# Optimization experiments

Hardware: AMD Instinct MI355X
Metric: run time of the kernel (lower is better)

Reference implementation:

```python
import jax, jax.numpy as jnp
import numpy as np

B, T, D_MODEL, N_HEAD = 2, 2048, 1024, 16
HEAD_DIM = D_MODEL // N_HEAD
CHUNK, POLY = 16, 1
SCALE = HEAD_DIM ** -0.5


def alpert_basis(L):
    # poly_order=1: constant + linear Legendre-like columns, L2-normalized per column
    t = jnp.linspace(-1.0, 1.0, L)
    W = jnp.stack([jnp.ones_like(t), t], axis=1)  # [L, 2]
    return W / jnp.linalg.norm(W, axis=0, keepdims=True)


def setup_inputs() -> dict:
    key = jax.random.key(0)
    ks = jax.random.split(key, 10)
    d = D_MODEL
    nrm = lambda k, shape, s=0.02: (jax.random.normal(k, shape, jnp.float32) * s)
    return {
        'x': jax.random.normal(ks[0], (B, T, d), jnp.float32),
        'Wq': nrm(ks[1], (d, d)),
        'Wk': nrm(ks[2], (d, d)),
        'Wv': nrm(ks[3], (d, d)),
        'Wo': nrm(ks[4], (d, d)),
        'gate_w': nrm(ks[5], (d, d)),
        'gate_b': jnp.zeros((d,), jnp.float32),
        'A': nrm(ks[6], (N_HEAD, HEAD_DIM, HEAD_DIM)),
        'jump_scale': jnp.ones((1,), jnp.float32),
        'jump_bias': jnp.zeros((1,), jnp.float32),
        'sink_scalar': nrm(ks[7], (1, N_HEAD, 1, 1)),
        'v_null': nrm(ks[8], (1, N_HEAD, 1, HEAD_DIM)),
    }


def _forward(x, Wq, Wk, Wv, Wo, gate_w, gate_b, A, jump_scale, jump_bias, sink_scalar, v_null):
    Bx, Tx, C = x.shape
    H, Dh = N_HEAD, HEAD_DIM
    NEG = jnp.float32(-1e30)

    def lin(W):  # torch Linear: y = x @ W.T, W is [out, in]
        y = jnp.einsum('btc,dc->btd', x, W)
        return y.reshape(Bx, Tx, H, Dh).transpose(0, 2, 1, 3)  # [B,H,T,Dh]

    q_raw, k_raw, v_val = lin(Wq), lin(Wk), lin(Wv)
    g = jax.nn.sigmoid(jnp.einsum('btc,dc->btd', x, gate_w) + gate_b)
    gate = g.reshape(Bx, Tx, H, Dh).transpose(0, 2, 1, 3)

    # symmetric mean/std normalization (torch std is unbiased -> ddof=1)
    ms = 0.5 * (q_raw.mean(-1, keepdims=True) + k_raw.mean(-1, keepdims=True))
    ss = 0.5 * (jnp.std(q_raw, -1, keepdims=True, ddof=1) + jnp.std(k_raw, -1, keepdims=True, ddof=1))
    q_norm = (q_raw - ms) / (ss + 1e-6)
    k_norm = (k_raw - ms) / (ss + 1e-6)

    # RoPE (half-split variant as in source)
    inv = 1.0 / (10000.0 ** (jnp.arange(0, Dh, 2, dtype=jnp.float32) / Dh))
    fr = jnp.arange(Tx, dtype=jnp.float32)[:, None] * inv[None, :]  # [T, Dh/2]
    cos, sin = jnp.cos(fr)[None, None], jnp.sin(fr)[None, None]

    def rope(z):
        z1, z2 = z[..., 0::2], z[..., 1::2]
        return jnp.concatenate([-z2 * sin + z1 * cos, z1 * sin + z2 * cos], axis=-1)

    S = A - jnp.swapaxes(A, -1, -2)  # skew-symmetric per head
    wedge = lambda z: z + jnp.einsum('bhtd,hde->bhte', z, S)
    q_geo, k_geo = wedge(rope(q_norm)), wedge(rope(k_norm))

    W_b = alpert_basis(CHUNK)  # [L, K]
    N, K, L = Tx // CHUNK, W_b.shape[1], CHUNK
    to_chunks = lambda z: z.reshape(Bx, H, N, L, Dh).transpose(2, 0, 1, 3, 4)  # [N,B,H,L,Dh]
    qx, kx, gx = to_chunks(q_geo), to_chunks(k_geo), to_chunks(gate)

    hist0 = jnp.zeros((Bx, H, N, K, Dh), jnp.float32)
    last0 = jnp.zeros((Bx, H, 1, Dh), jnp.float32)
    idx = jnp.arange(N)

    def step(carry, xs):
        hist, last, i = carry
        q_c, k_c, g_c = xs  # [B,H,L,Dh]
        k_coef = jnp.einsum('bhld,lk->bhkd', k_c, W_b)
        sc = jnp.einsum('bhkd,bhnkd->bhn', k_coef, hist) * SCALE
        sc = jnp.where(idx < i, sc, NEG)  # mask unfilled history slots
        w = jax.nn.softmax(sc, axis=-1)
        retr = jnp.einsum('bhn,bhnkd->bhkd', w, hist)
        q_rec = jnp.einsum('bhkd,lk->bhld', retr, W_b)
        jg = jax.nn.sigmoid(sc.max(-1)[..., None, None] * jump_scale + jump_bias)  # [B,H,1,1]
        inj = jnp.where(i > 0, (1.0 - jg) * last + jg * q_rec, 0.0)
        q_out = jnp.cumsum(g_c * q_c, axis=2) + inj
        hist = hist.at[:, :, i].set(jnp.einsum('bhld,lk->bhkd', q_out, W_b))
        return (hist, q_out[:, :, -1:, :], i + 1), q_out

    _, q_outs = jax.lax.scan(step, (hist0, last0, jnp.int32(0)), (qx, kx, gx))
    Q = q_outs.transpose(1, 2, 0, 3, 4).reshape(Bx, H, Tx, Dh)

    att = jnp.einsum('bhtd,bhsd->bhts', Q, k_geo) * SCALE
    causal = jnp.tril(jnp.ones((Tx, Tx), bool))
    att = jnp.where(causal, att, NEG)
    null = jnp.broadcast_to(sink_scalar, (Bx, H, Tx, 1))
    probs = jax.nn.softmax(jnp.concatenate([att, null], axis=-1), axis=-1)
    out = jnp.einsum('bhts,bhsd->bhtd', probs[..., :Tx], v_val) + probs[..., Tx:] * v_null
    out = out.transpose(0, 2, 1, 3).reshape(Bx, Tx, C)
    return jnp.einsum('btc,dc->btd', out, Wo)


def reference(x, Wq, Wk, Wv, Wo, gate_w, gate_b, A, jump_scale, jump_bias, sink_scalar, v_null):
    return _forward(x, Wq, Wk, Wv, Wo, gate_w, gate_b, A, jump_scale, jump_bias, sink_scalar, v_null)
```

## Files before the change

### kernel.cpp

```cpp
#include <hip/hip_runtime.h>
#include <math.h>

#define NB 2
#define NT 2048
#define NH 16
#define DH 64
#define DM 1024

using bf8   = __attribute__((ext_vector_type(8))) short;
using f32x4 = __attribute__((ext_vector_type(4))) float;

static __device__ __forceinline__ ushort f2bf(float f) {
    union { float f; unsigned u; } c; c.f = f;
    unsigned u = c.u + 0x7FFFu + ((c.u >> 16) & 1u);
    return (ushort)(u >> 16);
}

static __device__ __forceinline__ float wbf(int l, int k) {
    if (k == 0) return 0.25f;
    const float invn = 1.0f / sqrtf(1360.0f / 225.0f);
    return (-1.0f + (2.0f / 15.0f) * (float)l) * invn;
}

__global__ __launch_bounds__(512) void gemm3c_kernel(
    const float* __restrict__ x, const float* __restrict__ Wq,
    const float* __restrict__ Wk, const float* __restrict__ gw,
    const float* __restrict__ gbias,
    float* __restrict__ oq, float* __restrict__ ok, float* __restrict__ og,
    const float* __restrict__ wv, const float* __restrict__ wo,
    ushort* __restrict__ xb, ushort* __restrict__ wb)
{
    __shared__ float As[16][132];
    __shared__ float Bs[16][132];
    if (blockIdx.x >= 768) {
        const int id = (blockIdx.x - 768) * 512 + threadIdx.x;
        const int XQ = (NB * NT * DM) / 4;
        const int WQ = (DM * DM) / 4;
        const float4* src;
        ushort* dst;
        if (id < XQ) {
            src = (const float4*)x + id;
            dst = xb + (size_t)id * 4;
        } else {
            const int r = id - XQ;
            const int wi = r / WQ, off = r % WQ;
            const float* w = (wi == 0) ? wv : wo;
            src = (const float4*)w + off;
            dst = wb + (size_t)wi * DM * DM + (size_t)off * 4;
        }
        const float4 v = *src;
        ushort4 o;
        o.x = f2bf(v.x); o.y = f2bf(v.y); o.z = f2bf(v.z); o.w = f2bf(v.w);
        *(ushort4*)dst = o;
        return;
    }
    const int b = blockIdx.x;
    const int z = b >> 8;
    const int by = (b >> 3) & 31;
    const int bx = b & 7;
    const float* Bw = (z == 0) ? Wq : (z == 1) ? Wk : gw;
    float* C = (z == 0) ? oq : (z == 1) ? ok : og;
    const int tid = threadIdx.x;
    const int tx = tid & 31;
    const int ty = tid >> 5;
    const int row0 = by * 128, col0 = bx * 128;
    const int sr = tid >> 2;
    const int sk = (tid & 3) << 2;
    const float* Ap = x  + (size_t)(row0 + sr) * DM + sk;
    const float* Bp = Bw + (size_t)(col0 + sr) * DM + sk;
    float acc[8][4] = {};
    for (int k0 = 0; k0 < DM; k0 += 16) {
        const float4 av = *(const float4*)(Ap + k0);
        const float4 bv = *(const float4*)(Bp + k0);
        __syncthreads();
        As[sk + 0][sr] = av.x; As[sk + 1][sr] = av.y; As[sk + 2][sr] = av.z; As[sk + 3][sr] = av.w;
        Bs[sk + 0][sr] = bv.x; Bs[sk + 1][sr] = bv.y; Bs[sk + 2][sr] = bv.z; Bs[sk + 3][sr] = bv.w;
        __syncthreads();
        #pragma unroll
        for (int kk = 0; kk < 16; ++kk) {
            const float4 a0 = *(const float4*)&As[kk][ty * 4];
            const float4 a1 = *(const float4*)&As[kk][64 + ty * 4];
            const float4 b0 = *(const float4*)&Bs[kk][tx * 4];
            const float a[8] = {a0.x, a0.y, a0.z, a0.w, a1.x, a1.y, a1.z, a1.w};
            const float bb2[4] = {b0.x, b0.y, b0.z, b0.w};
            #pragma unroll
            for (int i = 0; i < 8; ++i)
                #pragma unroll
                for (int j = 0; j < 4; ++j)
                    acc[i][j] = fmaf(a[i], bb2[j], acc[i][j]);
        }
    }
    #pragma unroll
    for (int i = 0; i < 8; ++i) {
        const int m = row0 + ((i < 4) ? (ty * 4 + i) : (64 + ty * 4 + i - 4));
        const int bb = m >> 11, t = m & 2047;
        #pragma unroll
        for (int j = 0; j < 4; ++j) {
            const int n = col0 + tx * 4 + j;
            float v = acc[i][j];
            if (z == 2) v = 1.0f / (1.0f + __expf(-(v + gbias[n])));
            const int h = n >> 6, dh = n & 63;
            C[(((size_t)(bb * NH + h)) * NT + t) * DH + dh] = v;
        }
    }
}

__global__ __launch_bounds__(256) void gemm_bf16_kernel(
    const ushort* __restrict__ Ab, const ushort* __restrict__ Bb,
    float* __restrict__ Cp)
{
    __shared__ ushort Al[128][40];
    __shared__ ushort Bl[64][40];
    const int tid = threadIdx.x;
    const int l = tid & 63, w = tid >> 6;
    const int wr = w >> 1, wc = w & 1;
    const int lr = l & 15, g = l >> 4;
    const int row0 = blockIdx.y * 128, col0 = blockIdx.x * 64;
    f32x4 acc[4][2];
    #pragma unroll
    for (int mi = 0; mi < 4; ++mi)
        #pragma unroll
        for (int ni = 0; ni < 2; ++ni) acc[mi][ni] = (f32x4){0.f, 0.f, 0.f, 0.f};
    const int sa_row = tid >> 1, sa_half = (tid & 1) * 16;
    const int sb_row = tid >> 2, sb_q = (tid & 3) * 8;
    const ushort* Ap = Ab + (size_t)(row0 + sa_row) * DM + sa_half;
    const ushort* Bp = Bb + (size_t)(col0 + sb_row) * DM + sb_q;
    for (int k0 = 0; k0 < DM; k0 += 32) {
        const uint4 a0 = *(const uint4*)(Ap + k0);
        const uint4 a1 = *(const uint4*)(Ap + k0 + 8);
        const uint4 b0 = *(const uint4*)(Bp + k0);
        __syncthreads();
        *(uint4*)&Al[sa_row][sa_half]     = a0;
        *(uint4*)&Al[sa_row][sa_half + 8] = a1;
        *(uint4*)&Bl[sb_row][sb_q]        = b0;
        __syncthreads();
        bf8 a[4], b[2];
        #pragma unroll
        for (int mi = 0; mi < 4; ++mi) a[mi] = *(const bf8*)&Al[wr * 64 + mi * 16 + lr][g * 8];
        #pragma unroll
        for (int ni = 0; ni < 2; ++ni) b[ni] = *(const bf8*)&Bl[wc * 32 + ni * 16 + lr][g * 8];
        #pragma unroll
        for (int mi = 0; mi < 4; ++mi)
            #pragma unroll
            for (int ni = 0; ni < 2; ++ni)
                acc[mi][ni] = __builtin_amdgcn_mfma_f32_16x16x32_bf16(a[mi], b[ni], acc[mi][ni], 0, 0, 0);
    }
    #pragma unroll
    for (int mi = 0; mi < 4; ++mi) {
        const int m0 = row0 + wr * 64 + mi * 16 + g * 4;
        #pragma unroll
        for (int ni = 0; ni < 2; ++ni) {
            const int n = col0 + wc * 32 + ni * 16 + lr;
            #pragma unroll
            for (int r = 0; r < 4; ++r)
                Cp[(size_t)(m0 + r) * DM + n] = acc[mi][ni][r];
        }
    }
}

__global__ __launch_bounds__(256) void nrw_kernel(
    const float* __restrict__ qraw, const float* __restrict__ kraw,
    const float* __restrict__ Amat, float* __restrict__ gateq,
    ushort* __restrict__ kgb,
    float* __restrict__ kcoefA, float* __restrict__ R0A,
    float* __restrict__ R1A, float* __restrict__ r15A)
{
    __shared__ float S[64][64];
    __shared__ float zq[4][64];
    __shared__ float zk[4][64];
    const int bh = blockIdx.x;
    const int h = bh & (NH - 1);
    const int tid = threadIdx.x;
    const int g = tid >> 6, lane = tid & 63;
    for (int idx = tid; idx < 4096; idx += 256) {
        const int d = idx >> 6, e = idx & 63;
        S[d][e] = Amat[(size_t)h * 4096 + d * 64 + e] - Amat[(size_t)h * 4096 + e * 64 + d];
    }
    __syncthreads();
    const int j = lane & 31;
    const float invf = powf(10000.0f, -(float)(2 * j) * (1.0f / 64.0f));
    const int t0 = blockIdx.y * 64 + g * 16;
    float kc0 = 0.f, kc1 = 0.f, run = 0.f, Ra0 = 0.f, Ra1 = 0.f;
    for (int r = 0; r < 16; ++r) {
        const int t = t0 + r;
        const size_t base = ((size_t)bh * NT + t) * DH;
        const float qv = qraw[base + lane];
        const float kv = kraw[base + lane];
        float sq = qv, sk = kv, qq = qv * qv, kk2 = kv * kv;
        #pragma unroll
        for (int off = 32; off; off >>= 1) {
            sq += __shfl_xor(sq, off);
            sk += __shfl_xor(sk, off);
            qq += __shfl_xor(qq, off);
            kk2 += __shfl_xor(kk2, off);
        }
        const float mq = sq * (1.0f / 64.0f), mk = sk * (1.0f / 64.0f);
        const float vq = (qq - 64.0f * mq * mq) * (1.0f / 63.0f);
        const float vk = (kk2 - 64.0f * mk * mk) * (1.0f / 63.0f);
        const float ms = 0.5f * (mq + mk);
        const float ss = 0.5f * (sqrtf(fmaxf(vq, 0.0f)) + sqrtf(fmaxf(vk, 0.0f)));
        const float rinv = 1.0f / (ss + 1e-6f);
        const float qn = (qv - ms) * rinv;
        const float kn = (kv - ms) * rinv;
        const float q1 = __shfl(qn, 2 * j), q2 = __shfl(qn, 2 * j + 1);
        const float k1 = __shfl(kn, 2 * j), k2 = __shfl(kn, 2 * j + 1);
        float sn, cs;
        sincosf((float)t * invf, &sn, &cs);
        const float rq = (lane < 32) ? (q1 * cs - q2 * sn) : (q1 * sn + q2 * cs);
        const float rk = (lane < 32) ? (k1 * cs - k2 * sn) : (k1 * sn + k2 * cs);
        zq[g][lane] = rq;
        zk[g][lane] = rk;
        float aq = 0.0f, ak = 0.0f;
        #pragma unroll 8
        for (int d = 0; d < 64; ++d) {
            const float sde = S[d][lane];
            aq = fmaf(zq[g][d], sde, aq);
            ak = fmaf(zk[g][d], sde, ak);
        }
        const float qgv = rq + aq;
        const float kgv = rk + ak;
        const float gv = gateq[base + lane];
        const float qgpv = gv * qgv;
        gateq[base + lane] = qgpv;
        kgb[base + lane] = f2bf(kgv);
        kc0 = fmaf(kgv, 0.25f, kc0);
        kc1 = fmaf(kgv, wbf(r, 1), kc1);
        run += qgpv;
        Ra0 = fmaf(run, 0.25f, Ra0);
        Ra1 = fmaf(run, wbf(r, 1), Ra1);
    }
    const int unit = bh * 128 + blockIdx.y * 4 + g;
    kcoefA[(size_t)unit * 128 + lane] = kc0;
    kcoefA[(size_t)unit * 128 + 64 + lane] = kc1;
    R0A[(size_t)unit * 64 + lane] = Ra0;
    R1A[(size_t)unit * 64 + lane] = Ra1;
    r15A[(size_t)unit * 64 + lane] = run;
}

__global__ __launch_bounds__(256) void scan_vgemm_kernel(
    const float* __restrict__ kcoefA, const float* __restrict__ R0A,
    const float* __restrict__ R1A, const float* __restrict__ r15A,
    const float* __restrict__ jscale, const float* __restrict__ jbias,
    float* __restrict__ r0O, float* __restrict__ r1O,
    float* __restrict__ lpO, float* __restrict__ jgO,
    const ushort* __restrict__ xb, const ushort* __restrict__ Wb,
    ushort* __restrict__ Vt)
{
    __shared__ char smem[100864];
    if (blockIdx.x >= 32) {
        const int gi = blockIdx.x - 32;
        const int col0 = (gi & 15) * 64;
        const int row0 = (gi >> 4) * 128;
        ushort (*Al)[40] = (ushort(*)[40])smem;
        ushort (*Bl)[40] = (ushort(*)[40])(smem + 10240);
        const int tid = threadIdx.x;
        const int l = tid & 63, w = tid >> 6;
        const int wr = w >> 1, wc = w & 1;
        const int lr = l & 15, g = l >> 4;
        f32x4 acc[4][2];
        #pragma unroll
        for (int mi = 0; mi < 4; ++mi)
            #pragma unroll
            for (int ni = 0; ni < 2; ++ni) acc[mi][ni] = (f32x4){0.f, 0.f, 0.f, 0.f};
        const int sa_row = tid >> 1, sa_half = (tid & 1) * 16;
        const int sb_row = tid >> 2, sb_q = (tid & 3) * 8;
        const ushort* Ap = xb + (size_t)(row0 + sa_row) * DM + sa_half;
        const ushort* Bp = Wb + (size_t)(col0 + sb_row) * DM + sb_q;
        for (int k0 = 0; k0 < DM; k0 += 32) {
            const uint4 a0 = *(const uint4*)(Ap + k0);
            const uint4 a1 = *(const uint4*)(Ap + k0 + 8);
            const uint4 b0 = *(const uint4*)(Bp + k0);
            __syncthreads();
            *(uint4*)&Al[sa_row][sa_half]     = a0;
            *(uint4*)&Al[sa_row][sa_half + 8] = a1;
            *(uint4*)&Bl[sb_row][sb_q]        = b0;
            __syncthreads();
            bf8 a[4], b[2];
            #pragma unroll
            for (int mi = 0; mi < 4; ++mi) a[mi] = *(const bf8*)&Al[wr * 64 + mi * 16 + lr][g * 8];
            #pragma unroll
            for (int ni = 0; ni < 2; ++ni) b[ni] = *(const bf8*)&Bl[wc * 32 + ni * 16 + lr][g * 8];
            #pragma unroll
            for (int mi = 0; mi < 4; ++mi)
                #pragma unroll
                for (int ni = 0; ni < 2; ++ni)
                    acc[mi][ni] = __builtin_amdgcn_mfma_f32_16x16x32_bf16(a[mi], b[ni], acc[mi][ni], 0, 0, 0);
        }
        #pragma unroll
        for (int mi = 0; mi < 4; ++mi) {
            const int m0 = row0 + wr * 64 + mi * 16 + g * 4;
            const int bb = m0 >> 11, t0 = m0 & 2047;
            #pragma unroll
            for (int ni = 0; ni < 2; ++ni) {
                const int n = col0 + wc * 32 + ni * 16 + lr;
                const int h = n >> 6, dh = n & 63;
                ushort4 pk;
                pk.x = f2bf(acc[mi][ni][0]); pk.y = f2bf(acc[mi][ni][1]);
                pk.z = f2bf(acc[mi][ni][2]); pk.w = f2bf(acc[mi][ni][3]);
                *(ushort4*)(Vt + (((size_t)(bb * NH + h)) * DH + dh) * NT + t0) = pk;
            }
        }
        return;
    }
    if (threadIdx.x >= 64) return;
    float* HA  = (float*)smem;
    float* KcL = (float*)(smem + 65536);
    float* EL  = (float*)(smem + 73728);
    float* ET  = (float*)(smem + 82176);
    float* VP  = (float*)(smem + 92416);
    float* mxold = (float*)(smem + 100608);
    float* psold = (float*)(smem + 100672);
    float* pbuf  = (float*)(smem + 100736);
    float* qbuf    = (float*)(smem + 73728);
    float* candBuf = (float*)(smem + 74752);
    const int bh = blockIdx.x;
    const int l = threadIdx.x;
    #pragma unroll
    for (int c = 0; c < 64; ++c)
        *(f32x4*)&HA[c * 256 + l * 4] = (f32x4){0.f, 0.f, 0.f, 0.f};
    const float js = jscale[0], jb = jbias[0];
    const float* kcp  = kcoefA + (size_t)bh * 128 * 128;
    const float* R0p  = R0A  + (size_t)bh * 128 * 64;
    const float* R1p  = R1A  + (size_t)bh * 128 * 64;
    const float* r15p = r15A + (size_t)bh * 128 * 64;
    float* r0o = r0O + (size_t)bh * 128 * 64;
    float* r1o = r1O + (size_t)bh * 128 * 64;
    float* lpo = lpO + (size_t)bh * 128 * 64;
    float* jgo = jgO + (size_t)bh * 128;
    float last = 0.0f;
    const float wb15_1 = wbf(15, 1);
    const int iiq = l >> 2, sq = l & 3;
    const int ch = l >> 2;

    for (int j = 0; j < 8; ++j) {
        const int P = 16 * j;
        #pragma unroll
        for (int t = 0; t < 8; ++t)
            *(f32x4*)&KcL[t * 256 + l * 4] = *(const f32x4*)&kcp[j * 2048 + t * 256 + l * 4];
        float R0b[16], R1b[16], r15b[16];
        #pragma unroll
        for (int t = 0; t < 16; ++t) {
            R0b[t]  = R0p[(P + t) * 64 + l];
            R1b[t]  = R1p[(P + t) * 64 + l];
            r15b[t] = r15p[(P + t) * 64 + l];
        }
        {
            float sA[16], sB[16];
            #pragma unroll
            for (int ii = 0; ii < 16; ++ii) { sA[ii] = 0.f; sB[ii] = 0.f; }
            const int swA = l & 31;
            for (int c = 0; c < 32; ++c) {
                const int cs = ((c ^ swA) << 2);
                const f32x4 hA = *(const f32x4*)&HA[l * 128 + cs];
                const f32x4 hB = *(const f32x4*)&HA[(64 + l) * 128 + cs];
                #pragma unroll
                for (int ii = 0; ii < 16; ++ii) {
                    const f32x4 kc = *(const f32x4*)&KcL[ii * 128 + (c << 2)];
                    sA[ii] = fmaf(hA[0], kc[0], sA[ii]); sA[ii] = fmaf(hA[1], kc[1], sA[ii]);
                    sA[ii] = fmaf(hA[2], kc[2], sA[ii]); sA[ii] = fmaf(hA[3], kc[3], sA[ii]);
                    sB[ii] = fmaf(hB[0], kc[0], sB[ii]); sB[ii] = fmaf(hB[1], kc[1], sB[ii]);
                    sB[ii] = fmaf(hB[2], kc[2], sB[ii]); sB[ii] = fmaf(hB[3], kc[3], sB[ii]);
                }
            }
            #pragma unroll
            for (int ii = 0; ii < 16; ++ii) {
                if (l < P)      EL[ii * 132 + l]      = sA[ii] * 0.125f;
                if (64 + l < P) EL[ii * 132 + 64 + l] = sB[ii] * 0.125f;
            }
        }
        {
            float m = -1e30f;
            for (int n = sq; n < P; n += 4) m = fmaxf(m, EL[iiq * 132 + n]);
            m = fmaxf(m, __shfl_xor(m, 1));
            m = fmaxf(m, __shfl_xor(m, 2));
            if (sq == 0) mxold[iiq] = m;
        }
        {
            const float mo = (P > 0) ? mxold[iiq] : -1e30f;
            float ps = 0.f;
            for (int n = sq; n < P; n += 4) {
                const float e = __expf(EL[iiq * 132 + n] - mo);
                ET[n * 20 + iiq] = e;
                ps += e;
            }
            ps += __shfl_xor(ps, 1);
            ps += __shfl_xor(ps, 2);
            if (sq == 0) psold[iiq] = ps;
        }
        {
            float vp0[16], vp1[16];
            #pragma unroll
            for (int ii = 0; ii < 16; ++ii) { vp0[ii] = 0.f; vp1[ii] = 0.f; }
            for (int n = 0; n < P; ++n) {
                const int sw = n & 31;
                const float h0 = HA[n * 128 + ((ch ^ sw) << 2) + (l & 3)];
                const float h1 = HA[n * 128 + (((16 + ch) ^ sw) << 2) + (l & 3)];
                const f32x4 e0 = *(const f32x4*)&ET[n * 20];
                const f32x4 e1 = *(const f32x4*)&ET[n * 20 + 4];
                const f32x4 e2 = *(const f32x4*)&ET[n * 20 + 8];
                const f32x4 e3 = *(const f32x4*)&ET[n * 20 + 12];
                #pragma unroll
                for (int u = 0; u < 4; ++u) {
                    vp0[u]      = fmaf(e0[u], h0, vp0[u]);      vp1[u]      = fmaf(e0[u], h1, vp1[u]);
                    vp0[4 + u]  = fmaf(e1[u], h0, vp0[4 + u]);  vp1[4 + u]  = fmaf(e1[u], h1, vp1[4 + u]);
                    vp0[8 + u]  = fmaf(e2[u], h0, vp0[8 + u]);  vp1[8 + u]  = fmaf(e2[u], h1, vp1[8 + u]);
                    vp0[12 + u] = fmaf(e3[u], h0, vp0[12 + u]); vp1[12 + u] = fmaf(e3[u], h1, vp1[12 + u]);
                }
            }
            #pragma unroll
            for (int ii = 0; ii < 16; ++ii) {
                VP[ii * 128 + l]      = vp0[ii];
                VP[ii * 128 + 64 + l] = vp1[ii];
            }
        }
        const int n_ = l >> 2, q = l & 3;
        const int qb = l & ~3;
        #pragma unroll
        for (int iL = 0; iL < 16; ++iL) {
            const int i = P + iL;
            const int nrow = P + n_;
            const int nsw = nrow & 31;
            float scp = 0.f;
            #pragma unroll
            for (int c = 0; c < 8; ++c) {
                const f32x4 h  = *(const f32x4*)&HA[nrow * 128 + ((((q << 3) + c) ^ nsw) << 2)];
                const f32x4 kc = *(const f32x4*)&KcL[iL * 128 + (q << 5) + (c << 2)];
                scp = fmaf(h[0], kc[0], scp); scp = fmaf(h[1], kc[1], scp);
                scp = fmaf(h[2], kc[2], scp); scp = fmaf(h[3], kc[3], scp);
            }
            qbuf[l] = scp;
            const float scn = (qbuf[qb] + qbuf[qb + 1]) + (qbuf[qb + 2] + qbuf[qb + 3]);
            const float cand = (n_ < iL) ? scn * 0.125f : -1e30f;
            if (q == 0) candBuf[n_] = cand;
            float m8[8];
            #pragma unroll
            for (int u = 0; u < 8; ++u) m8[u] = fmaxf(candBuf[2 * u], candBuf[2 * u + 1]);
            float m4a = fmaxf(m8[0], m8[1]), m4b = fmaxf(m8[2], m8[3]);
            float m4c = fmaxf(m8[4], m8[5]), m4d = fmaxf(m8[6], m8[7]);
            const float mxn = fmaxf(fmaxf(m4a, m4b), fmaxf(m4c, m4d));
            const float mo = mxold[iL];
            const float mx = fmaxf(mxn, mo);
            const float p = (n_ < iL) ? __expf(cand - mx) : 0.f;
            if (q == 0) pbuf[n_] = p;
            float s8[8];
            #pragma unroll
            for (int u = 0; u < 8; ++u) s8[u] = pbuf[2 * u] + pbuf[2 * u + 1];
            float s4a = s8[0] + s8[1], s4b = s8[2] + s8[3];
            float s4c = s8[4] + s8[5], s4d = s8[6] + s8[7];
            const float psn = (s4a + s4b) + (s4c + s4d);
            float r0 = 0.f, r1 = 0.f;
            if (i > 0) {
                const float so = __expf(mo - mx);
                float racc0 = VP[iL * 128 + l] * so;
                float racc1 = VP[iL * 128 + 64 + l] * so;
                #pragma unroll
                for (int n2 = 0; n2 < iL; ++n2) {
                    const float pn = pbuf[n2];
                    const int nr = P + n2;
                    const int sw2 = nr & 31;
                    racc0 = fmaf(pn, HA[nr * 128 + ((ch ^ sw2) << 2) + (l & 3)], racc0);
                    racc1 = fmaf(pn, HA[nr * 128 + (((16 + ch) ^ sw2) << 2) + (l & 3)], racc1);
                }
                const float ps = fmaf(psold[iL], so, psn);
                const float rden = 1.0f / ps;
                r0 = racc0 * rden;
                r1 = racc1 * rden;
            }
            const float jg = 1.0f / (1.0f + __expf(-fmaf(mx, js, jb)));
            const float lastp = last;
            const float h0n = R0b[iL] + fmaf(jg, r0, 4.0f * (1.0f - jg) * lastp);
            const float h1n = fmaf(jg, r1, R1b[iL]);
            const float qrec15 = fmaf(r0, 0.25f, r1 * wb15_1);
            last = r15b[iL] + fmaf(jg, qrec15, (1.0f - jg) * lastp);
            r0o[i * 64 + l] = r0;
            r1o[i * 64 + l] = r1;
            lpo[i * 64 + l] = lastp;
            if (l == 0) jgo[i] = jg;
            const int swi = i & 31;
            HA[i * 128 + ((ch ^ swi) << 2) + (l & 3)] = h0n;
            HA[i * 128 + (((16 + ch) ^ swi) << 2) + (l & 3)] = h1n;
        }
    }
}

__global__ __launch_bounds__(256) void scan_post_kernel(
    const float* __restrict__ qgp, const float* __restrict__ r0O,
    const float* __restrict__ r1O, const float* __restrict__ lpO,
    const float* __restrict__ jgO, float* __restrict__ Qout)
{
    const int unit = blockIdx.x * 4 + (threadIdx.x >> 6);
    const int d = threadIdx.x & 63;
    const int bh = unit >> 7, i = unit & 127;
    const size_t ub = (size_t)unit * 64 + d;
    const float r0 = r0O[ub], r1 = r1O[ub], lp = lpO[ub];
    const float jg = jgO[unit];
    const size_t cbase = ((size_t)bh * NT + i * 16) * DH + d;
    float run = 0.0f;
    #pragma unroll
    for (int ll = 0; ll < 16; ++ll) {
        run += qgp[cbase + ll * 64];
        const float qrec = fmaf(r0, 0.25f, r1 * wbf(ll, 1));
        const float inj = (i > 0) ? fmaf(jg, qrec, (1.0f - jg) * lp) : 0.0f;
        Qout[cbase + ll * 64] = run + inj;
    }
}

__global__ __launch_bounds__(256) void attn_mfma_kernel(
    const float* __restrict__ Qf, const ushort* __restrict__ Kb,
    const ushort* __restrict__ Vtb, const float* __restrict__ sink,
    const float* __restrict__ vnull, ushort* __restrict__ Ob)
{
    __shared__ ushort Kl0[64][40], Kl1[64][40];
    __shared__ ushort Vl0[64][40], Vl1[64][40];
    __shared__ ushort Pl[4][2][16][40];
    const int bh = blockIdx.y;
    const int h = bh & (NH - 1);
    const int b = bh >> 4;
    const int qt = gridDim.x - 1 - blockIdx.x;
    const int q0 = qt * 64;
    const int tid = threadIdx.x;
    const int w = tid >> 6, l = tid & 63;
    const int lr = l & 15, g = l >> 4;
    bf8 qf[2];
    {
        const float* qp = Qf + (((size_t)bh * NT) + q0 + 16 * w + lr) * DH + g * 8;
        #pragma unroll
        for (int ks = 0; ks < 2; ++ks) {
            const float4 f0 = *(const float4*)(qp + 32 * ks);
            const float4 f1 = *(const float4*)(qp + 32 * ks + 4);
            bf8 q;
            q[0] = (short)f2bf(f0.x); q[1] = (short)f2bf(f0.y);
            q[2] = (short)f2bf(f0.z); q[3] = (short)f2bf(f0.w);
            q[4] = (short)f2bf(f1.x); q[5] = (short)f2bf(f1.y);
            q[6] = (short)f2bf(f1.z); q[7] = (short)f2bf(f1.w);
            qf[ks] = q;
        }
    }
    f32x4 oacc[4];
    #pragma unroll
    for (int nf2 = 0; nf2 < 4; ++nf2) oacc[nf2] = (f32x4){0.f, 0.f, 0.f, 0.f};
    float mrow[4], lrowp[4];
    #pragma unroll
    for (int r = 0; r < 4; ++r) { mrow[r] = -1e30f; lrowp[r] = 0.0f; }
    const int ntiles = qt + 1;
    const ushort* Kg = Kb + (size_t)bh * NT * DH;
    const ushort* Vg = Vtb + (size_t)bh * DH * NT;
    const int srow = tid >> 2;
    const int sc16 = (tid & 3) * 16;
    for (int it = 0; it < ntiles; ++it) {
        const int kv0 = it * 64;
        __syncthreads();
        {
            const ushort* kp = Kg + (size_t)(kv0 + srow) * DH + sc16;
            const ushort* vp = Vg + (size_t)srow * NT + kv0 + sc16;
            ushort* kd = (sc16 < 32) ? &Kl0[srow][sc16] : &Kl1[srow][sc16 - 32];
            ushort* vd = (sc16 < 32) ? &Vl0[srow][sc16] : &Vl1[srow][sc16 - 32];
            *(uint4*)kd       = *(const uint4*)kp;
            *(uint4*)(kd + 8) = *(const uint4*)(kp + 8);
            *(uint4*)vd       = *(const uint4*)vp;
            *(uint4*)(vd + 8) = *(const uint4*)(vp + 8);
        }
        __syncthreads();
        f32x4 s[4];
        #pragma unroll
        for (int nf = 0; nf < 4; ++nf) {
            s[nf] = (f32x4){0.f, 0.f, 0.f, 0.f};
            const bf8 kf0 = *(const bf8*)&Kl0[nf * 16 + lr][g * 8];
            const bf8 kf1 = *(const bf8*)&Kl1[nf * 16 + lr][g * 8];
            s[nf] = __builtin_amdgcn_mfma_f32_16x16x32_bf16(qf[0], kf0, s[nf], 0, 0, 0);
            s[nf] = __builtin_amdgcn_mfma_f32_16x16x32_bf16(qf[1], kf1, s[nf], 0, 0, 0);
        }
        #pragma unroll
        for (int r = 0; r < 4; ++r) {
            const int row = q0 + 16 * w + g * 4 + r;
            float sv[4];
            float tmax = -1e30f;
            #pragma unroll
            for (int nf = 0; nf < 4; ++nf) {
                const int col = kv0 + nf * 16 + lr;
                sv[nf] = (col <= row) ? s[nf][r] * 0.125f : -1e30f;
                tmax = fmaxf(tmax, sv[nf]);
            }
            tmax = fmaxf(tmax, __shfl_xor(tmax, 1));
            tmax = fmaxf(tmax, __shfl_xor(tmax, 2));
            tmax = fmaxf(tmax, __shfl_xor(tmax, 4));
            tmax = fmaxf(tmax, __shfl_xor(tmax, 8));
            const float mnew = fmaxf(mrow[r], tmax);
            const float csc = __expf(mrow[r] - mnew);
            float plocal = 0.f;
            #pragma unroll
            for (int nf = 0; nf < 4; ++nf) {
                const float p = __expf(sv[nf] - mnew);
                plocal += p;
                Pl[w][nf >> 1][g * 4 + r][(nf & 1) * 16 + lr] = f2bf(p);
            }
            lrowp[r] = lrowp[r] * csc + plocal;
            mrow[r] = mnew;
            #pragma unroll
            for (int nf2 = 0; nf2 < 4; ++nf2) oacc[nf2][r] *= csc;
        }
        const bf8 pa0 = *(const bf8*)&Pl[w][0][lr][g * 8];
        const bf8 pa1 = *(const bf8*)&Pl[w][1][lr][g * 8];
        #pragma unroll
        for (int nf2 = 0; nf2 < 4; ++nf2) {
            const bf8 vb0 = *(const bf8*)&Vl0[nf2 * 16 + lr][g * 8];
            const bf8 vb1 = *(const bf8*)&Vl1[nf2 * 16 + lr][g * 8];
            oacc[nf2] = __builtin_amdgcn_mfma_f32_16x16x32_bf16(pa0, vb0, oacc[nf2], 0, 0, 0);
            oacc[nf2] = __builtin_amdgcn_mfma_f32_16x16x32_bf16(pa1, vb1, oacc[nf2], 0, 0, 0);
        }
    }
    float lrow[4];
    #pragma unroll
    for (int r = 0; r < 4; ++r) {
        float ps = lrowp[r];
        ps += __shfl_xor(ps, 1);
        ps += __shfl_xor(ps, 2);
        ps += __shfl_xor(ps, 4);
        ps += __shfl_xor(ps, 8);
        lrow[r] = ps;
    }
    const float s0 = sink[h];
    float c0v[4], pnv[4], rden[4];
    #pragma unroll
    for (int r = 0; r < 4; ++r) {
        const float mf = fmaxf(mrow[r], s0);
        c0v[r] = __expf(mrow[r] - mf);
        pnv[r] = __expf(s0 - mf);
        rden[r] = 1.0f / fmaf(lrow[r], c0v[r], pnv[r]);
    }
    #pragma unroll
    for (int nf2 = 0; nf2 < 4; ++nf2) {
        const float vn = vnull[h * DH + nf2 * 16 + lr];
        #pragma unroll
        for (int r = 0; r < 4; ++r) {
            const float out = fmaf(pnv[r], vn, oacc[nf2][r] * c0v[r]) * rden[r];
            const int trow = q0 + 16 * w + g * 4 + r;
            Ob[(((size_t)b * NT) + trow) * DM + h * DH + nf2 * 16 + lr] = f2bf(out);
        }
    }
}

extern "C" void kernel_launch(void* const* d_in, const int* in_sizes, int n_in,
                              void* d_out, int out_size, void* d_ws, size_t ws_size,
                              hipStream_t stream) {
    const float* x     = (const float*)d_in[0];
    const float* Wq    = (const float*)d_in[1];
    const float* Wk    = (const float*)d_in[2];
    const float* Wv    = (const float*)d_in[3];
    const float* Wo    = (const float*)d_in[4];
    const float* gw    = (const float*)d_in[5];
    const float* gbias = (const float*)d_in[6];
    const float* Amat  = (const float*)d_in[7];
    const float* js    = (const float*)d_in[8];
    const float* jb    = (const float*)d_in[9];
    const float* sink  = (const float*)d_in[10];
    const float* vnull = (const float*)d_in[11];
    char* ws = (char*)d_ws;
    const size_t MB = 1024 * 1024;
    float*  q_raw  = (float*)(ws + 0);
    float*  k_raw  = (float*)(ws + 16 * MB);
    float*  gate   = (float*)(ws + 32 * MB);
    ushort* kgb    = (ushort*)(ws + 64 * MB);
    ushort* xb     = (ushort*)(ws + 72 * MB);
    ushort* Wb     = (ushort*)(ws + 80 * MB);
    float*  kcoefA = (float*)(ws + 84 * MB);
    float*  R0A    = (float*)(ws + 86 * MB);
    float*  R1A    = (float*)(ws + 87 * MB);
    float*  r15A   = (float*)(ws + 88 * MB);
    float*  r0O    = (float*)(ws + 89 * MB);
    float*  r1O    = (float*)(ws + 90 * MB);
    float*  lpO    = (float*)(ws + 91 * MB);
    float*  jgO    = (float*)(ws + 92 * MB);
    ushort* Vt     = (ushort*)k_raw;
    ushort* attob  = (ushort*)(ws + 24 * MB);

    gemm3c_kernel<<<3840, 512, 0, stream>>>(
        x, Wq, Wk, gw, gbias, q_raw, k_raw, gate, Wv, Wo, xb, Wb);
    nrw_kernel<<<dim3(NB * NH, NT / 64), 256, 0, stream>>>(
        q_raw, k_raw, Amat, gate, kgb, kcoefA, R0A, R1A, r15A);
    scan_vgemm_kernel<<<32 + 512, 256, 0, stream>>>(
        kcoefA, R0A, R1A, r15A, js, jb, r0O, r1O, lpO, jgO, xb, Wb, Vt);
    scan_post_kernel<<<1024, 256, 0, stream>>>(gate, r0O, r1O, lpO, jgO, q_raw);
    attn_mfma_kernel<<<dim3(NT / 64, NB * NH), 256, 0, stream>>>(q_raw, kgb, Vt, sink, vnull, attob);
    gemm_bf16_kernel<<<dim3(DM / 64, (NB * NT) / 128), 256, 0, stream>>>(
        attob, Wb + DM * DM, (float*)d_out);
}
```

Before: 797.6 us.

## Replace FP32 QKG projection GEMM with split-bf16 MFMA emulation

The FP32 FMA GEMM for the Q, K and gate projections is replaced by a kernel that splits each fp32 operand into three bf16 parts (high, mid, low) and accumulates six bf16 MFMA products, giving near-fp32 accuracy on the matrix cores. The bf16 cast of x, Wv and Wo, which was fused into the GEMM launch, moves into its own kernel launched first. This trades the scalar FMA throughput limit for extra conversion work and six times the MFMA count, plus one more kernel launch.

```diff
diff --git a/kernel.cpp b/kernel.cpp
--- a/kernel.cpp
+++ b/kernel.cpp
@@ -15,6 +15,10 @@
     unsigned u = c.u + 0x7FFFu + ((c.u >> 16) & 1u);
     return (ushort)(u >> 16);
 }
+static __device__ __forceinline__ float bf2f(ushort u) {
+    union { unsigned u; float f; } c; c.u = ((unsigned)u) << 16;
+    return c.f;
+}
 
 static __device__ __forceinline__ float wbf(int l, int k) {
     if (k == 0) return 0.25f;
@@ -22,85 +26,143 @@
     return (-1.0f + (2.0f / 15.0f) * (float)l) * invn;
 }
 
-__global__ __launch_bounds__(512) void gemm3c_kernel(
+__global__ __launch_bounds__(256) void cast3_kernel(
+    const float* __restrict__ x, const float* __restrict__ wv,
+    const float* __restrict__ wo, ushort* __restrict__ xb, ushort* __restrict__ wb)
+{
+    const int id = blockIdx.x * 256 + threadIdx.x;
+    const int XQ = (NB * NT * DM) / 4;
+    const int WQ = (DM * DM) / 4;
+    const float4* src;
+    ushort* dst;
+    if (id < XQ) {
+        src = (const float4*)x + id;
+        dst = xb + (size_t)id * 4;
+    } else {
+        const int r = id - XQ;
+        const int wi = r / WQ, off = r % WQ;
+        const float* w = (wi == 0) ? wv : wo;
+        src = (const float4*)w + off;
+        dst = wb + (size_t)wi * DM * DM + (size_t)off * 4;
+    }
+    const float4 v = *src;
+    ushort4 o;
+    o.x = f2bf(v.x); o.y = f2bf(v.y); o.z = f2bf(v.z); o.w = f2bf(v.w);
+    *(ushort4*)dst = o;
+}
+
+__global__ __launch_bounds__(256) void gemm3m_kernel(
     const float* __restrict__ x, const float* __restrict__ Wq,
     const float* __restrict__ Wk, const float* __restrict__ gw,
     const float* __restrict__ gbias,
-    float* __restrict__ oq, float* __restrict__ ok, float* __restrict__ og,
-    const float* __restrict__ wv, const float* __restrict__ wo,
-    ushort* __restrict__ xb, ushort* __restrict__ wb)
+    float* __restrict__ oq, float* __restrict__ ok, float* __restrict__ og)
 {
-    __shared__ float As[16][132];
-    __shared__ float Bs[16][132];
-    if (blockIdx.x >= 768) {
-        const int id = (blockIdx.x - 768) * 512 + threadIdx.x;
-        const int XQ = (NB * NT * DM) / 4;
-        const int WQ = (DM * DM) / 4;
-        const float4* src;
-        ushort* dst;
-        if (id < XQ) {
-            src = (const float4*)x + id;
-            dst = xb + (size_t)id * 4;
-        } else {
-            const int r = id - XQ;
-            const int wi = r / WQ, off = r % WQ;
-            const float* w = (wi == 0) ? wv : wo;
-            src = (const float4*)w + off;
-            dst = wb + (size_t)wi * DM * DM + (size_t)off * 4;
-        }
-        const float4 v = *src;
-        ushort4 o;
-        o.x = f2bf(v.x); o.y = f2bf(v.y); o.z = f2bf(v.z); o.w = f2bf(v.w);
-        *(ushort4*)dst = o;
-        return;
-    }
-    const int b = blockIdx.x;
-    const int z = b >> 8;
-    const int by = (b >> 3) & 31;
-    const int bx = b & 7;
+    __shared__ ushort Ah[128][40], Am[128][40], Al[128][40];
+    __shared__ ushort Bh[64][40],  Bm[64][40],  Bl[64][40];
+    const int z = blockIdx.z;
     const float* Bw = (z == 0) ? Wq : (z == 1) ? Wk : gw;
     float* C = (z == 0) ? oq : (z == 1) ? ok : og;
     const int tid = threadIdx.x;
-    const int tx = tid & 31;
-    const int ty = tid >> 5;
-    const int row0 = by * 128, col0 = bx * 128;
-    const int sr = tid >> 2;
-    const int sk = (tid & 3) << 2;
-    const float* Ap = x  + (size_t)(row0 + sr) * DM + sk;
-    const float* Bp = Bw + (size_t)(col0 + sr) * DM + sk;
-    float acc[8][4] = {};
-    for (int k0 = 0; k0 < DM; k0 += 16) {
-        const float4 av = *(const float4*)(Ap + k0);
-        const float4 bv = *(const float4*)(Bp + k0);
+    const int l = tid & 63, w = tid >> 6;
+    const int wr = w >> 1, wc = w & 1;
+    const int lr = l & 15, g = l >> 4;
+    const int row0 = blockIdx.y * 128, col0 = blockIdx.x * 64;
+    f32x4 acc[4][2];
+    #pragma unroll
+    for (int mi = 0; mi < 4; ++mi)
+        #pragma unroll
+        for (int ni = 0; ni < 2; ++ni) acc[mi][ni] = (f32x4){0.f, 0.f, 0.f, 0.f};
+    const int sa_row = tid >> 1, sa_col = (tid & 1) * 16;
+    const int sb_row = tid >> 2, sb_col = (tid & 3) * 8;
+    const float* Ap = x  + (size_t)(row0 + sa_row) * DM + sa_col;
+    const float* Bp = Bw + (size_t)(col0 + sb_row) * DM + sb_col;
+    for (int k0 = 0; k0 < DM; k0 += 32) {
+        float av[16], bv[8];
+        *(float4*)&av[0]  = *(const float4*)(Ap + k0);
+        *(float4*)&av[4]  = *(const float4*)(Ap + k0 + 4);
+        *(float4*)&av[8]  = *(const float4*)(Ap + k0 + 8);
+        *(float4*)&av[12] = *(const float4*)(Ap + k0 + 12);
+        *(float4*)&bv[0]  = *(const float4*)(Bp + k0);
+        *(float4*)&bv[4]  = *(const float4*)(Bp + k0 + 4);
         __syncthreads();
-        As[sk + 0][sr] = av.x; As[sk + 1][sr] = av.y; As[sk + 2][sr] = av.z; As[sk + 3][sr] = av.w;
-        Bs[sk + 0][sr] = bv.x; Bs[sk + 1][sr] = bv.y; Bs[sk + 2][sr] = bv.z; Bs[sk + 3][sr] = bv.w;
+        #pragma unroll
+        for (int c = 0; c < 16; c += 4) {
+            ushort4 hh, mm, ll;
+            ushort* hp = (ushort*)&hh;
+            ushort* mp = (ushort*)&mm;
+            ushort* lp = (ushort*)&ll;
+            #pragma unroll
+            for (int u = 0; u < 4; ++u) {
+                const float v = av[c + u];
+                const ushort hu = f2bf(v);
+                const float r1 = v - bf2f(hu);
+                const ushort mu = f2bf(r1);
+                const ushort lu = f2bf(r1 - bf2f(mu));
+                hp[u] = hu; mp[u] = mu; lp[u] = lu;
+            }
+            *(ushort4*)&Ah[sa_row][sa_col + c] = hh;
+            *(ushort4*)&Am[sa_row][sa_col + c] = mm;
+            *(ushort4*)&Al[sa_row][sa_col + c] = ll;
+        }
+        #pragma unroll
+        for (int c = 0; c < 8; c += 4) {
+            ushort4 hh, mm, ll;
+            ushort* hp = (ushort*)&hh;
+            ushort* mp = (ushort*)&mm;
+            ushort* lp = (ushort*)&ll;
+            #pragma unroll
+            for (int u = 0; u < 4; ++u) {
+                const float v = bv[c + u];
+                const ushort hu = f2bf(v);
+                const float r1 = v - bf2f(hu);
+                const ushort mu = f2bf(r1);
+                const ushort lu = f2bf(r1 - bf2f(mu));
+                hp[u] = hu; mp[u] = mu; lp[u] = lu;
+            }
+            *(ushort4*)&Bh[sb_row][sb_col + c] = hh;
+            *(ushort4*)&Bm[sb_row][sb_col + c] = mm;
+            *(ushort4*)&Bl[sb_row][sb_col + c] = ll;
+        }
         __syncthreads();
-        #pragma unroll
-        for (int kk = 0; kk < 16; ++kk) {
-            const float4 a0 = *(const float4*)&As[kk][ty * 4];
-            const float4 a1 = *(const float4*)&As[kk][64 + ty * 4];
-            const float4 b0 = *(const float4*)&Bs[kk][tx * 4];
-            const float a[8] = {a0.x, a0.y, a0.z, a0.w, a1.x, a1.y, a1.z, a1.w};
-            const float bb2[4] = {b0.x, b0.y, b0.z, b0.w};
-            #pragma unroll
-            for (int i = 0; i < 8; ++i)
-                #pragma unroll
-                for (int j = 0; j < 4; ++j)
-                    acc[i][j] = fmaf(a[i], bb2[j], acc[i][j]);
-        }
-    }
-    #pragma unroll
-    for (int i = 0; i < 8; ++i) {
-        const int m = row0 + ((i < 4) ? (ty * 4 + i) : (64 + ty * 4 + i - 4));
-        const int bb = m >> 11, t = m & 2047;
-        #pragma unroll
-        for (int j = 0; j < 4; ++j) {
-            const int n = col0 + tx * 4 + j;
-            float v = acc[i][j];
-            if (z == 2) v = 1.0f / (1.0f + __expf(-(v + gbias[n])));
+        bf8 ah[4], am[4], al[4], bh[2], bm[2], bl[2];
+        #pragma unroll
+        for (int mi = 0; mi < 4; ++mi) {
+            ah[mi] = *(const bf8*)&Ah[wr * 64 + mi * 16 + lr][g * 8];
+            am[mi] = *(const bf8*)&Am[wr * 64 + mi * 16 + lr][g * 8];
+            al[mi] = *(const bf8*)&Al[wr * 64 + mi * 16 + lr][g * 8];
+        }
+        #pragma unroll
+        for (int ni = 0; ni < 2; ++ni) {
+            bh[ni] = *(const bf8*)&Bh[wc * 32 + ni * 16 + lr][g * 8];
+            bm[ni] = *(const bf8*)&Bm[wc * 32 + ni * 16 + lr][g * 8];
+            bl[ni] = *(const bf8*)&Bl[wc * 32 + ni * 16 + lr][g * 8];
+        }
+        #pragma unroll
+        for (int mi = 0; mi < 4; ++mi)
+            #pragma unroll
+            for (int ni = 0; ni < 2; ++ni) {
+                acc[mi][ni] = __builtin_amdgcn_mfma_f32_16x16x32_bf16(ah[mi], bh[ni], acc[mi][ni], 0, 0, 0);
+                acc[mi][ni] = __builtin_amdgcn_mfma_f32_16x16x32_bf16(ah[mi], bm[ni], acc[mi][ni], 0, 0, 0);
+                acc[mi][ni] = __builtin_amdgcn_mfma_f32_16x16x32_bf16(am[mi], bh[ni], acc[mi][ni], 0, 0, 0);
+                acc[mi][ni] = __builtin_amdgcn_mfma_f32_16x16x32_bf16(am[mi], bm[ni], acc[mi][ni], 0, 0, 0);
+                acc[mi][ni] = __builtin_amdgcn_mfma_f32_16x16x32_bf16(ah[mi], bl[ni], acc[mi][ni], 0, 0, 0);
+                acc[mi][ni] = __builtin_amdgcn_mfma_f32_16x16x32_bf16(al[mi], bh[ni], acc[mi][ni], 0, 0, 0);
+            }
+    }
+    #pragma unroll
+    for (int mi = 0; mi < 4; ++mi) {
+        const int m0 = row0 + wr * 64 + mi * 16 + g * 4;
+        const int bb = m0 >> 11, t0 = m0 & 2047;
+        #pragma unroll
+        for (int ni = 0; ni < 2; ++ni) {
+            const int n = col0 + wc * 32 + ni * 16 + lr;
             const int h = n >> 6, dh = n & 63;
-            C[(((size_t)(bb * NH + h)) * NT + t) * DH + dh] = v;
+            #pragma unroll
+            for (int r = 0; r < 4; ++r) {
+                float v = acc[mi][ni][r];
+                if (z == 2) v = 1.0f / (1.0f + __expf(-(v + gbias[n])));
+                C[(((size_t)(bb * NH + h)) * NT + (t0 + r)) * DH + dh] = v;
+            }
         }
     }
 }
@@ -674,8 +736,9 @@
     ushort* Vt     = (ushort*)k_raw;
     ushort* attob  = (ushort*)(ws + 24 * MB);
 
-    gemm3c_kernel<<<3840, 512, 0, stream>>>(
-        x, Wq, Wk, gw, gbias, q_raw, k_raw, gate, Wv, Wo, xb, Wb);
+    cast3_kernel<<<6144, 256, 0, stream>>>(x, Wv, Wo, xb, Wb);
+    gemm3m_kernel<<<dim3(DM / 64, (NB * NT) / 128, 3), 256, 0, stream>>>(
+        x, Wq, Wk, gw, gbias, q_raw, k_raw, gate);
     nrw_kernel<<<dim3(NB * NH, NT / 64), 256, 0, stream>>>(
         q_raw, k_raw, Amat, gate, kgb, kcoefA, R0A, R1A, r15A);
     scan_vgemm_kernel<<<32 + 512, 256, 0, stream>>>(
```

After: 664.0 us (median of 4 runs). 16.7% less time.
